# Kernel optimization log

Measured on AMD Instinct MI355X. Metric: run time of the kernel, lower is better.

Reference implementation:

```python
import jax, jax.numpy as jnp
import numpy as np

N, E, D_IN, HD, H = 50000, 800000, 768, 64, 4
HC = HD * H


def _gat(x, src, dst, etypes, lin_w, att_src, att_dst, edge_emb, lin_edge_w, att_edge,
         bias, res_w, res_b, ln_g, ln_b):
    # Faithful PyG GATConv (edge_dim, concat=True, add_self_loops=True with
    # fill_value='mean', negative_slope=0.2) + residual + LayerNorm. Eval mode: no dropout.
    n = x.shape[0]
    h, c = att_src.shape
    xs = (x @ lin_w).reshape(n, h, c)                      # [N,H,C]
    a_src = jnp.einsum('nhc,hc->nh', xs, att_src)          # [N,H]
    a_dst = jnp.einsum('nhc,hc->nh', xs, att_dst)
    eattr = edge_emb[etypes]                               # [E,ed]
    ones = jnp.ones((etypes.shape[0],), x.dtype)
    cnt = jax.ops.segment_sum(ones, dst, num_segments=n)
    # self-loop edge_attr = mean of incoming edge attrs per node (fill_value='mean')
    loop_attr = jax.ops.segment_sum(eattr, dst, num_segments=n) / jnp.maximum(cnt, 1.0)[:, None]
    loop = jnp.arange(n, dtype=src.dtype)
    src_a = jnp.concatenate([src, loop])
    dst_a = jnp.concatenate([dst, loop])
    e_all = jnp.concatenate([eattr, loop_attr], 0)
    a_edge = jnp.einsum('ehc,hc->eh', (e_all @ lin_edge_w).reshape(-1, h, c), att_edge)
    alpha = jax.nn.leaky_relu(a_src[src_a] + a_dst[dst_a] + a_edge, 0.2)   # [Ea,H]
    # edge softmax over incoming edges of each destination node
    amax = jax.ops.segment_max(alpha, dst_a, num_segments=n)
    ea = jnp.exp(alpha - amax[dst_a])
    denom = jax.ops.segment_sum(ea, dst_a, num_segments=n)
    w = ea / (denom[dst_a] + 1e-16)
    out = jax.ops.segment_sum(xs[src_a] * w[:, :, None], dst_a, num_segments=n)
    out = out.reshape(n, h * c) + bias + (x @ res_w + res_b)
    mu = out.mean(-1, keepdims=True)
    var = jnp.mean((out - mu) ** 2, -1, keepdims=True)
    return (out - mu) * jax.lax.rsqrt(var + 1e-5) * ln_g + ln_b


def _forward(features, positions,
             fe_w1, fe_b1, fe_w2, fe_b2, fe_pos_w, fe_pos_b, fe_type_emb, fe_out_w, fe_out_b,
             g1_lin_w, g1_att_src, g1_att_dst, g1_edge_emb, g1_lin_edge_w, g1_att_edge,
             g1_bias, g1_res_w, g1_res_b, g1_ln_g, g1_ln_b,
             g2_lin_w, g2_att_src, g2_att_dst, g2_edge_emb, g2_lin_edge_w, g2_att_edge,
             g2_bias, g2_res_w, g2_res_b, g2_ln_g, g2_ln_b,
             cls_w, cls_b,
             edge_index, aspect_indices, edge_types, node_types):
    # EnhancedFeatureExtractor (eval: dropout = identity)
    hfe = jax.nn.relu(features @ fe_w1 + fe_b1) @ fe_w2 + fe_b2
    hfe = hfe + fe_type_emb[node_types] + positions[:, None] @ fe_pos_w + fe_pos_b
    hfe = hfe @ fe_out_w + fe_out_b
    src, dst = edge_index[0], edge_index[1]
    hid = _gat(hfe, src, dst, edge_types, g1_lin_w, g1_att_src, g1_att_dst, g1_edge_emb,
               g1_lin_edge_w, g1_att_edge, g1_bias, g1_res_w, g1_res_b, g1_ln_g, g1_ln_b)
    hid = jax.nn.relu(hid)
    hid = _gat(hid, src, dst, edge_types, g2_lin_w, g2_att_src, g2_att_dst, g2_edge_emb,
               g2_lin_edge_w, g2_att_edge, g2_bias, g2_res_w, g2_res_b, g2_ln_g, g2_ln_b)
    return hid[aspect_indices] @ cls_w + cls_b


def setup_inputs() -> dict:
    key = jax.random.key(0)
    ks = jax.random.split(key, 40)
    d = {}
    d['features'] = jax.random.normal(ks[0], (N, D_IN), jnp.float32)
    d['edge_index'] = jax.random.randint(ks[1], (2, E), 0, N, jnp.int32)
    d['aspect_indices'] = jax.random.randint(ks[2], (4096,), 0, N, jnp.int32)
    d['edge_types'] = jax.random.randint(ks[3], (E,), 0, 4, jnp.int32)
    d['node_types'] = jax.random.randint(ks[4], (N,), 0, 3, jnp.int32)
    d['positions'] = jax.random.uniform(ks[5], (N,), jnp.float32)

    def rn(i, shape, s=0.05):
        return s * jax.random.normal(ks[i], shape, jnp.float32)

    d['fe_w1'] = rn(6, (D_IN, HD)); d['fe_b1'] = rn(7, (HD,))
    d['fe_w2'] = rn(8, (HD, HD));   d['fe_b2'] = rn(9, (HD,))
    d['fe_pos_w'] = rn(10, (1, HD)); d['fe_pos_b'] = rn(11, (HD,))
    d['fe_type_emb'] = rn(12, (3, HD))
    d['fe_out_w'] = rn(13, (HD, HD)); d['fe_out_b'] = rn(14, (HD,))
    d['g1_lin_w'] = rn(15, (HD, HC))
    d['g1_att_src'] = rn(16, (H, HD)); d['g1_att_dst'] = rn(17, (H, HD))
    d['g1_edge_emb'] = rn(18, (4, 4)); d['g1_lin_edge_w'] = rn(19, (4, HC))
    d['g1_att_edge'] = rn(20, (H, HD))
    d['g1_bias'] = rn(21, (HC,)); d['g1_res_w'] = rn(22, (HD, HC)); d['g1_res_b'] = rn(23, (HC,))
    d['g1_ln_g'] = jnp.ones((HC,), jnp.float32); d['g1_ln_b'] = jnp.zeros((HC,), jnp.float32)
    d['g2_lin_w'] = rn(24, (HC, HD))
    d['g2_att_src'] = rn(25, (1, HD)); d['g2_att_dst'] = rn(26, (1, HD))
    d['g2_edge_emb'] = rn(27, (4, 4)); d['g2_lin_edge_w'] = rn(28, (4, HD))
    d['g2_att_edge'] = rn(29, (1, HD))
    d['g2_bias'] = rn(30, (HD,)); d['g2_res_w'] = rn(31, (HC, HD)); d['g2_res_b'] = rn(32, (HD,))
    d['g2_ln_g'] = jnp.ones((HD,), jnp.float32); d['g2_ln_b'] = jnp.zeros((HD,), jnp.float32)
    d['cls_w'] = rn(33, (HD, 3)); d['cls_b'] = rn(34, (3,))
    return d


def reference(features, edge_index, aspect_indices, edge_types, node_types, positions,
              fe_w1, fe_b1, fe_w2, fe_b2, fe_pos_w, fe_pos_b, fe_type_emb, fe_out_w, fe_out_b,
              g1_lin_w, g1_att_src, g1_att_dst, g1_edge_emb, g1_lin_edge_w, g1_att_edge,
              g1_bias, g1_res_w, g1_res_b, g1_ln_g, g1_ln_b,
              g2_lin_w, g2_att_src, g2_att_dst, g2_edge_emb, g2_lin_edge_w, g2_att_edge,
              g2_bias, g2_res_w, g2_res_b, g2_ln_g, g2_ln_b,
              cls_w, cls_b):
    return _forward(features, positions,
                    fe_w1, fe_b1, fe_w2, fe_b2, fe_pos_w, fe_pos_b, fe_type_emb, fe_out_w, fe_out_b,
                    g1_lin_w, g1_att_src, g1_att_dst, g1_edge_emb, g1_lin_edge_w, g1_att_edge,
                    g1_bias, g1_res_w, g1_res_b, g1_ln_g, g1_ln_b,
                    g2_lin_w, g2_att_src, g2_att_dst, g2_edge_emb, g2_lin_edge_w, g2_att_edge,
                    g2_bias, g2_res_w, g2_res_b, g2_ln_g, g2_ln_b,
                    cls_w, cls_b,
                    edge_index, aspect_indices, edge_types, node_types)
```

## Files before the change

kernel.cpp:

```cpp
#include <hip/hip_runtime.h>


#define LRELU(x) ((x) > 0.f ? (x) : 0.2f * (x))

typedef __attribute__((ext_vector_type(8))) short short8;
typedef __attribute__((ext_vector_type(4))) float floatx4;

__device__ __forceinline__ unsigned short f2bf(float x) {
    union { float f; unsigned int u; } v; v.f = x;
    unsigned int r = (v.u + 0x7FFFu + ((v.u >> 16) & 1u)) >> 16;
    return (unsigned short)r;
}
__device__ __forceinline__ unsigned int cvtpk(float lo, float hi) {
    unsigned int r;
    asm("v_cvt_pk_bf16_f32 %0, %1, %2" : "=v"(r) : "v"(lo), "v"(hi));
    return r;
}
__device__ __forceinline__ float bflo(unsigned int u) {
    return __uint_as_float(u << 16);
}
__device__ __forceinline__ float bfhi(unsigned int u) {
    return __uint_as_float(u & 0xFFFF0000u);
}
__device__ __forceinline__ float bf1(unsigned short u) {
    return __uint_as_float(((unsigned int)u) << 16);
}

__global__ __launch_bounds__(256) void k_pre0(
    const float* __restrict__ e_emb1, const float* __restrict__ lew1,
    const float* __restrict__ ae1,
    const float* __restrict__ e_emb2, const float* __restrict__ lew2,
    const float* __restrict__ ae2,
    float* __restrict__ aet1, float* __restrict__ aet2,
    const float* __restrict__ w2, const float* __restrict__ outw,
    const float* __restrict__ b2, const float* __restrict__ posb,
    const float* __restrict__ outb, const float* __restrict__ temb,
    const float* __restrict__ posw,
    float* __restrict__ W2p, float* __restrict__ h0,
    float* __restrict__ tadd, float* __restrict__ padd)
{
    __shared__ float M1[16];
    __shared__ float M2[4];
    int t = threadIdx.x;
    if (blockIdx.x == 0) {
        if (t < 16) {
            int d = t >> 2, h = t & 3;
            float s = 0.f;
            for (int c = 0; c < 64; ++c) s += lew1[d * 256 + h * 64 + c] * ae1[h * 64 + c];
            M1[d * 4 + h] = s;
        }
        if (t < 4) {
            float s = 0.f;
            for (int c = 0; c < 64; ++c) s += lew2[t * 64 + c] * ae2[c];
            M2[t] = s;
        }
        __syncthreads();
        if (t < 16) {
            int ty = t >> 2, h = t & 3;
            float s = 0.f;
            for (int d = 0; d < 4; ++d) s += e_emb1[ty * 4 + d] * M1[d * 4 + h];
            aet1[ty * 4 + h] = s;
        }
        if (t < 4) {
            float s = 0.f;
            for (int d = 0; d < 4; ++d) s += e_emb2[t * 4 + d] * M2[d];
            aet2[t] = s;
        }
    } else {
        int i = t >> 2, jq = (t & 3) * 16;
        float a16[16];
#pragma unroll
        for (int u = 0; u < 16; ++u) a16[u] = 0.f;
        for (int k = 0; k < 64; ++k) {
            float a = w2[i * 64 + k];
            const float* op = outw + k * 64 + jq;
            float4 o0 = *(const float4*)op;
            float4 o1 = *(const float4*)(op + 4);
            float4 o2 = *(const float4*)(op + 8);
            float4 o3 = *(const float4*)(op + 12);
            a16[0] += a * o0.x;  a16[1] += a * o0.y;  a16[2] += a * o0.z;  a16[3] += a * o0.w;
            a16[4] += a * o1.x;  a16[5] += a * o1.y;  a16[6] += a * o1.z;  a16[7] += a * o1.w;
            a16[8] += a * o2.x;  a16[9] += a * o2.y;  a16[10] += a * o2.z; a16[11] += a * o2.w;
            a16[12] += a * o3.x; a16[13] += a * o3.y; a16[14] += a * o3.z; a16[15] += a * o3.w;
        }
#pragma unroll
        for (int u = 0; u < 16; ++u) W2p[i * 64 + jq + u] = a16[u];
        for (int e = t; e < 320; e += 256) {
            int g = e >> 6, j = e & 63;
            float s = 0.f;
            for (int k = 0; k < 64; ++k) {
                float v;
                if (g == 0) v = b2[k] + posb[k];
                else if (g <= 3) v = temb[(g - 1) * 64 + k];
                else v = posw[k];
                s += v * outw[k * 64 + j];
            }
            if (g == 0) h0[j] = s + outb[j];
            else if (g <= 3) tadd[(g - 1) * 64 + j] = s;
            else padd[j] = s;
        }
    }
}

__global__ __launch_bounds__(256) void k_bswz(
    const float* __restrict__ w1, const float* __restrict__ B1,
    const float* __restrict__ B2,
    unsigned short* __restrict__ out_fe1, unsigned short* __restrict__ out_p2)
{
    int idx = blockIdx.x * 256 + threadIdx.x;
    if (idx < 768 * 64) {
        int k = idx >> 6, col = idx & 63;
        int c = k >> 6, kl = k & 63, kg = kl >> 3, j = kl & 7;
        out_fe1[((c * 8 + kg) * 64 + col) * 8 + j] = f2bf(w1[k * 64 + col]);
    } else {
        int i2 = idx - 768 * 64;
        int k = i2 >> 7, col = i2 & 127;
        float v = (col < 64) ? B1[k * 64 + col] : B2[k * 64 + col - 64];
        int c = k >> 6, kl = k & 63, kg = kl >> 3, j = kl & 7;
        out_p2[((c * 8 + kg) * 128 + col) * 8 + j] = f2bf(v);
    }
}

__global__ __launch_bounds__(64) void k_fuse2(
    const float* __restrict__ W2p, const float* __restrict__ h0,
    const float* __restrict__ tadd, const float* __restrict__ padd,
    const float* __restrict__ lin_w, const float* __restrict__ res_w,
    const float* __restrict__ bias, const float* __restrict__ res_b,
    unsigned short* __restrict__ bz, float* __restrict__ C0,
    float* __restrict__ T, float* __restrict__ P)
{
    __shared__ float bcol[64];
    int c = blockIdx.x;
    int j = threadIdx.x;
    int cL = c & 255;
    const float* Bsrc = (c < 256) ? lin_w : res_w;
    float bv = Bsrc[j * 256 + cL];
    bcol[j] = bv;
    __syncthreads();
    float s = 0.f;
#pragma unroll 8
    for (int k = 0; k < 64; ++k) s += W2p[j * 64 + k] * bcol[k];
    int kg = j >> 3, jj = j & 7, ct = c >> 7, cl = c & 127;
    bz[((ct * 8 + kg) * 128 + cl) * 8 + jj] = f2bf(s);
    float pc = h0[j] * bv;
    float p0 = tadd[j] * bv, p1 = tadd[64 + j] * bv, p2 = tadd[128 + j] * bv;
    float pp = padd[j] * bv;
#pragma unroll
    for (int k = 32; k; k >>= 1) {
        pc += __shfl_xor(pc, k, 64); p0 += __shfl_xor(p0, k, 64);
        p1 += __shfl_xor(p1, k, 64); p2 += __shfl_xor(p2, k, 64);
        pp += __shfl_xor(pp, k, 64);
    }
    if (j == 0) {
        C0[c] = pc + ((c >= 256) ? (bias[cL] + res_b[cL]) : 0.f);
        T[c] = p0; T[512 + c] = p1; T[1024 + c] = p2;
        P[c] = pp;
    }
}

__global__ __launch_bounds__(256) void k_fe1(
    const float* __restrict__ feat, const unsigned short* __restrict__ bswz,
    const float* __restrict__ b1, unsigned short* __restrict__ t1b, int N)
{
    int t = threadIdx.x;
    int wv = t >> 6, lane = t & 63;
    int quad = lane >> 4, l16 = lane & 15;
    long rw = (long)blockIdx.x * 64 + wv * 16;
    long ra = rw + l16;
    if (ra >= N) ra = N - 1;
    const float* fbase = feat + ra * 768 + quad * 8;

    floatx4 acc[4];
#pragma unroll
    for (int i = 0; i < 4; ++i) acc[i] = (floatx4){0.f, 0.f, 0.f, 0.f};

    for (int ci = 0; ci < 12; ++ci) {
        const float* fc = fbase + ci * 64;
        short8 af[2];
#pragma unroll
        for (int s = 0; s < 2; ++s) {
            float4 x = *(const float4*)(fc + s * 32);
            float4 y = *(const float4*)(fc + s * 32 + 4);
            uint4 u = {cvtpk(x.x, x.y), cvtpk(x.z, x.w),
                       cvtpk(y.x, y.y), cvtpk(y.z, y.w)};
            af[s] = *(short8*)&u;
        }
#pragma unroll
        for (int s = 0; s < 2; ++s) {
            int kg = s * 4 + quad;
#pragma unroll
            for (int ct = 0; ct < 4; ++ct) {
                short8 bfrag = *(const short8*)&bswz[
                    ((ci * 8 + kg) * 64 + ct * 16 + l16) * 8];
                acc[ct] = __builtin_amdgcn_mfma_f32_16x16x32_bf16(
                    af[s], bfrag, acc[ct], 0, 0, 0);
            }
        }
    }
#pragma unroll
    for (int ct = 0; ct < 4; ++ct) {
        float bb = b1[ct * 16 + l16];
#pragma unroll
        for (int r = 0; r < 4; ++r) {
            long m = rw + quad * 4 + r;
            if (m < N)
                t1b[m * 64 + ct * 16 + l16] = f2bf(fmaxf(acc[ct][r] + bb, 0.f));
        }
    }
}

__global__ __launch_bounds__(256) void k_prep1(
    const unsigned short* __restrict__ A, const unsigned short* __restrict__ bswz,
    const float* __restrict__ C0, const float* __restrict__ T,
    const float* __restrict__ P, const int* __restrict__ ntypes,
    const float* __restrict__ pos,
    unsigned short* __restrict__ xsb, unsigned short* __restrict__ resp, int N)
{
    int t = threadIdx.x;
    int wv = t >> 6, lane = t & 63;
    int quad = lane >> 4, l16 = lane & 15;
    long rw = (long)blockIdx.x * 64 + wv * 16;
    int by = blockIdx.y;
    long ra = rw + l16;
    if (ra >= N) ra = N - 1;
    const unsigned short* abase = A + ra * 64 + quad * 8;

    floatx4 acc[8];
#pragma unroll
    for (int i = 0; i < 8; ++i) acc[i] = (floatx4){0.f, 0.f, 0.f, 0.f};

    short8 af[2];
    af[0] = *(const short8*)(abase);
    af[1] = *(const short8*)(abase + 32);
#pragma unroll
    for (int s = 0; s < 2; ++s) {
        int kg = s * 4 + quad;
#pragma unroll
        for (int c8 = 0; c8 < 8; ++c8) {
            short8 bfrag = *(const short8*)&bswz[
                ((by * 8 + kg) * 128 + c8 * 16 + l16) * 8];
            acc[c8] = __builtin_amdgcn_mfma_f32_16x16x32_bf16(
                af[s], bfrag, acc[c8], 0, 0, 0);
        }
    }
    int nta[4];
    float posa[4];
#pragma unroll
    for (int r = 0; r < 4; ++r) {
        long m = rw + quad * 4 + r;
        if (m < N) { nta[r] = ntypes[m]; posa[r] = pos[m]; }
        else       { nta[r] = 0; posa[r] = 0.f; }
    }
    bool isl = (by < 2);
    int cb = by * 128;
#pragma unroll
    for (int c8 = 0; c8 < 8; ++c8) {
        int gc = cb + c8 * 16 + l16;
        float c0 = C0[gc], pcf = P[gc];
#pragma unroll
        for (int r = 0; r < 4; ++r) {
            long m = rw + quad * 4 + r;
            if (m < N) {
                float val = acc[c8][r] + c0 + T[nta[r] * 512 + gc] + posa[r] * pcf;
                if (isl) xsb[m * 256 + gc] = f2bf(val);
                else     resp[m * 256 + gc - 256] = f2bf(val);
            }
        }
    }
}

__global__ __launch_bounds__(256) void k_prep2(
    const unsigned short* __restrict__ A, const unsigned short* __restrict__ bswz,
    const float* __restrict__ bias, const float* __restrict__ res_b,
    unsigned short* __restrict__ xsb, float* __restrict__ resp, int N)
{
    int t = threadIdx.x;
    int wv = t >> 6, lane = t & 63;
    int quad = lane >> 4, l16 = lane & 15;
    long rw = (long)blockIdx.x * 64 + wv * 16;
    long ra = rw + l16;
    if (ra >= N) ra = N - 1;
    const unsigned short* abase = A + ra * 256 + quad * 8;

    floatx4 acc[8];
#pragma unroll
    for (int i = 0; i < 8; ++i) acc[i] = (floatx4){0.f, 0.f, 0.f, 0.f};

    for (int ci = 0; ci < 4; ++ci) {
        short8 af[2];
        af[0] = *(const short8*)(abase + ci * 64);
        af[1] = *(const short8*)(abase + ci * 64 + 32);
#pragma unroll
        for (int s = 0; s < 2; ++s) {
            int kg = s * 4 + quad;
#pragma unroll
            for (int c8 = 0; c8 < 8; ++c8) {
                short8 bfrag = *(const short8*)&bswz[
                    ((ci * 8 + kg) * 128 + c8 * 16 + l16) * 8];
                acc[c8] = __builtin_amdgcn_mfma_f32_16x16x32_bf16(
                    af[s], bfrag, acc[c8], 0, 0, 0);
            }
        }
    }
#pragma unroll
    for (int c8 = 0; c8 < 8; ++c8) {
        int gc = c8 * 16 + l16;
        bool isl = gc < 64;
        float badd = isl ? 0.f : (bias[gc - 64] + res_b[gc - 64]);
#pragma unroll
        for (int r = 0; r < 4; ++r) {
            long m = rw + quad * 4 + r;
            if (m < N) {
                float val = acc[c8][r];
                if (isl) xsb[m * 64 + gc] = f2bf(val);
                else     resp[m * 64 + gc - 64] = val + badd;
            }
        }
    }
}

template<int H>
__global__ __launch_bounds__(256) void k_att(
    const unsigned short* __restrict__ xsb, const float* __restrict__ att_s,
    const float* __restrict__ att_d, float* __restrict__ a_src,
    float* __restrict__ a_dst, int N)
{
    int t = threadIdx.x;
    int wv = t >> 6, lane = t & 63;
    long n = (long)blockIdx.x * 4 + wv;
    if (n >= N) return;
    if (H == 4) {
        ushort4 u = *(const ushort4*)&xsb[n * 256 + lane * 4];
        float4 as = *(const float4*)&att_s[lane * 4];
        float4 ad = *(const float4*)&att_d[lane * 4];
        float x0 = bf1(u.x), x1 = bf1(u.y), x2 = bf1(u.z), x3 = bf1(u.w);
        float p = x0 * as.x + x1 * as.y + x2 * as.z + x3 * as.w;
        float q = x0 * ad.x + x1 * ad.y + x2 * ad.z + x3 * ad.w;
#pragma unroll
        for (int k = 8; k; k >>= 1) {
            p += __shfl_xor(p, k, 64);
            q += __shfl_xor(q, k, 64);
        }
        if ((lane & 15) == 0) {
            a_src[n * 4 + (lane >> 4)] = p;
            a_dst[n * 4 + (lane >> 4)] = q;
        }
    } else {
        float x = bf1(xsb[n * 64 + lane]);
        float p = x * att_s[lane];
        float q = x * att_d[lane];
#pragma unroll
        for (int k = 32; k; k >>= 1) {
            p += __shfl_xor(p, k, 64);
            q += __shfl_xor(q, k, 64);
        }
        if (lane == 0) { a_src[n] = p; a_dst[n] = q; }
    }
}

__global__ __launch_bounds__(256) void k_count(
    const int* __restrict__ dst, const int* __restrict__ et,
    int* __restrict__ cnt_t, int E)
{
    int e = blockIdx.x * 256 + threadIdx.x;
    if (e < E) atomicAdd(&cnt_t[dst[e] * 4 + et[e]], 1);
}

__global__ __launch_bounds__(256) void k_scan1(
    const int* __restrict__ cnt_t, int* __restrict__ row_off,
    int* __restrict__ blk_sums, int N)
{
    __shared__ int s[256];
    int t = threadIdx.x;
    int i = blockIdx.x * 256 + t;
    int v = 0;
    if (i < N) v = cnt_t[4 * i] + cnt_t[4 * i + 1] + cnt_t[4 * i + 2] + cnt_t[4 * i + 3];
    s[t] = v;
    __syncthreads();
    for (int off = 1; off < 256; off <<= 1) {
        int x = 0;
        if (t >= off) x = s[t - off];
        __syncthreads();
        s[t] += x;
        __syncthreads();
    }
    if (i < N) row_off[i] = s[t] - v;
    if (t == 255) blk_sums[blockIdx.x] = s[255];
}

__global__ __launch_bounds__(256) void k_scan2(int* __restrict__ blk_sums, int nb)
{
    __shared__ int s[256];
    int t = threadIdx.x;
    int v = (t < nb) ? blk_sums[t] : 0;
    s[t] = v;
    __syncthreads();
    for (int off = 1; off < 256; off <<= 1) {
        int x = 0;
        if (t >= off) x = s[t - off];
        __syncthreads();
        s[t] += x;
        __syncthreads();
    }
    if (t < nb) blk_sums[t] = s[t] - v;
}

__global__ __launch_bounds__(256) void k_scan3(
    int* __restrict__ row_off, int* __restrict__ cursor,
    const int* __restrict__ blk_sums, int N, int E)
{
    int t = threadIdx.x;
    int i = blockIdx.x * 256 + t;
    if (i < N) {
        int o = row_off[i] + blk_sums[blockIdx.x];
        row_off[i] = o;
        cursor[i] = o;
    }
    if (i == 0) row_off[N] = E;
}

__global__ __launch_bounds__(256) void k_scatter(
    const int* __restrict__ src, const int* __restrict__ dst,
    const int* __restrict__ et, int* __restrict__ cursor,
    int* __restrict__ csr_pack, int E)
{
    int e = blockIdx.x * 256 + threadIdx.x;
    if (e < E) {
        int d = dst[e];
        int pos = atomicAdd(&cursor[d], 1);
        csr_pack[pos] = src[e] | (et[e] << 28);
    }
}

__global__ __launch_bounds__(128) void k_gat1(
    const unsigned short* __restrict__ xs1b, const float* __restrict__ a_src,
    const float* __restrict__ a_dst, const int* __restrict__ row_off,
    const int* __restrict__ csr_pack,
    const int* __restrict__ cnt_t, const float* __restrict__ aet1,
    const float* __restrict__ ln_g, const float* __restrict__ ln_b,
    const unsigned short* __restrict__ res, unsigned short* __restrict__ out)
{
    __shared__ __align__(16) float4 ws[2][64];
    __shared__ float2 aetp[2][4];
    __shared__ float red[4];
    int n = blockIdx.x;
    int t = threadIdx.x;
    int w = t >> 6, c = t & 63;
    int lc = c & 15, g = c >> 4;
    int h0 = 2 * w;
    if (t < 8) {
        int w2 = t >> 2, ty = t & 3;
        aetp[w2][ty] = make_float2(aet1[ty * 4 + 2 * w2], aet1[ty * 4 + 2 * w2 + 1]);
    }
    int off = row_off[n], deg = row_off[n + 1] - off;
    float2 a_d = *(const float2*)&a_dst[n * 4 + h0];
    __syncthreads();
    float ael0 = 0.f, ael1 = 0.f;
    int degc = 0;
#pragma unroll
    for (int ty = 0; ty < 4; ++ty) {
        int ct = cnt_t[n * 4 + ty];
        degc += ct;
        float2 ae = aetp[w][ty];
        ael0 += (float)ct * ae.x;
        ael1 += (float)ct * ae.y;
    }
    float inv = (degc > 0) ? 1.f / (float)degc : 1.f;
    float2 a_s_self = *(const float2*)&a_src[n * 4 + h0];
    float al0 = a_s_self.x + a_d.x + ael0 * inv;
    float al1 = a_s_self.y + a_d.y + ael1 * inv;
    al0 = LRELU(al0); al1 = LRELU(al1);
    float wself0 = expf(al0), wself1 = expf(al1);

    int col0 = w * 128 + lc * 8;
    const unsigned short* xrow = xs1b + col0;
    float acc[8];
#pragma unroll
    for (int j = 0; j < 8; ++j) acc[j] = 0.f;
    float dp0 = 0.f, dp1 = 0.f;

    for (int base = 0; base < deg; base += 64) {
        int cnt = min(64, deg - base);
        float w0 = 0.f, w1 = 0.f;
        int s = 0;
        if (c < cnt) {
            int pk = csr_pack[off + base + c];
            s = pk & 0x0FFFFFFF;
            int ty = ((unsigned)pk) >> 28;
            float2 as2 = *(const float2*)&a_src[s * 4 + h0];
            float2 ae = aetp[w][ty];
            float a0 = as2.x + a_d.x + ae.x;
            float a1 = as2.y + a_d.y + ae.y;
            a0 = LRELU(a0); a1 = LRELU(a1);
            w0 = expf(a0); w1 = expf(a1);
        }
        dp0 += w0; dp1 += w1;
        ws[w][c] = make_float4(w0, w1, __int_as_float(s), 0.f);
        int cr = (cnt + 7) & ~7;
        for (int i = 0; i < cr; i += 8) {
#pragma unroll
            for (int u = 0; u < 2; ++u) {
                float4 p = ws[w][i + u * 4 + g];
                float wl = (lc < 8) ? p.x : p.y;
                uint4 q = *(const uint4*)&xrow[(long)__float_as_int(p.z) * 256];
                acc[0] += wl * bflo(q.x); acc[1] += wl * bfhi(q.x);
                acc[2] += wl * bflo(q.y); acc[3] += wl * bfhi(q.y);
                acc[4] += wl * bflo(q.z); acc[5] += wl * bfhi(q.z);
                acc[6] += wl * bflo(q.w); acc[7] += wl * bfhi(q.w);
            }
        }
    }
#pragma unroll
    for (int k = 32; k; k >>= 1) {
        dp0 += __shfl_xor(dp0, k, 64);
        dp1 += __shfl_xor(dp1, k, 64);
    }
#pragma unroll
    for (int j = 0; j < 8; ++j) {
        acc[j] += __shfl_xor(acc[j], 16, 64);
        acc[j] += __shfl_xor(acc[j], 32, 64);
    }
    uint4 us = *(const uint4*)&xrow[(long)n * 256];
    float wself_l = (lc < 8) ? wself0 : wself1;
    acc[0] += wself_l * bflo(us.x); acc[1] += wself_l * bfhi(us.x);
    acc[2] += wself_l * bflo(us.y); acc[3] += wself_l * bfhi(us.y);
    acc[4] += wself_l * bflo(us.z); acc[5] += wself_l * bfhi(us.z);
    acc[6] += wself_l * bflo(us.w); acc[7] += wself_l * bfhi(us.w);
    float dsum = ((lc < 8) ? dp0 + wself0 : dp1 + wself1) + 1e-16f;
    float rd = 1.f / dsum;
    uint4 ur = *(const uint4*)&res[(long)n * 256 + col0];
    float v[8];
    v[0] = acc[0] * rd + bflo(ur.x); v[1] = acc[1] * rd + bfhi(ur.x);
    v[2] = acc[2] * rd + bflo(ur.y); v[3] = acc[3] * rd + bfhi(ur.y);
    v[4] = acc[4] * rd + bflo(ur.z); v[5] = acc[5] * rd + bfhi(ur.z);
    v[6] = acc[6] * rd + bflo(ur.w); v[7] = acc[7] * rd + bfhi(ur.w);
    float s1 = 0.f, s2 = 0.f;
#pragma unroll
    for (int j = 0; j < 8; ++j) { s1 += v[j]; s2 += v[j] * v[j]; }
#pragma unroll
    for (int k = 32; k; k >>= 1) {
        s1 += __shfl_xor(s1, k, 64);
        s2 += __shfl_xor(s2, k, 64);
    }
    if (c == 0) { red[w] = s1 * 0.25f; red[2 + w] = s2 * 0.25f; }
    __syncthreads();
    float mu = (red[0] + red[1]) * (1.f / 256.f);
    float var = (red[2] + red[3]) * (1.f / 256.f) - mu * mu;
    float rs = rsqrtf(var + 1e-5f);
    if (g == 0) {
        float4 lg0 = *(const float4*)&ln_g[col0];
        float4 lg1 = *(const float4*)&ln_g[col0 + 4];
        float4 lb0 = *(const float4*)&ln_b[col0];
        float4 lb1 = *(const float4*)&ln_b[col0 + 4];
        float y[8];
        y[0] = fmaxf((v[0] - mu) * rs * lg0.x + lb0.x, 0.f);
        y[1] = fmaxf((v[1] - mu) * rs * lg0.y + lb0.y, 0.f);
        y[2] = fmaxf((v[2] - mu) * rs * lg0.z + lb0.z, 0.f);
        y[3] = fmaxf((v[3] - mu) * rs * lg0.w + lb0.w, 0.f);
        y[4] = fmaxf((v[4] - mu) * rs * lg1.x + lb1.x, 0.f);
        y[5] = fmaxf((v[5] - mu) * rs * lg1.y + lb1.y, 0.f);
        y[6] = fmaxf((v[6] - mu) * rs * lg1.z + lb1.z, 0.f);
        y[7] = fmaxf((v[7] - mu) * rs * lg1.w + lb1.w, 0.f);
        uint4 o;
        o.x = cvtpk(y[0], y[1]); o.y = cvtpk(y[2], y[3]);
        o.z = cvtpk(y[4], y[5]); o.w = cvtpk(y[6], y[7]);
        *(uint4*)&out[(long)n * 256 + col0] = o;
    }
}

__global__ __launch_bounds__(64) void k_gat2(
    const unsigned short* __restrict__ xs2b, const float* __restrict__ a_src,
    const float* __restrict__ a_dst, const int* __restrict__ row_off,
    const int* __restrict__ csr_pack,
    const int* __restrict__ cnt_t, const float* __restrict__ aet2,
    const float* __restrict__ ln_g, const float* __restrict__ ln_b,
    float* io)
{
    __shared__ __align__(8) float2 ws[64];
    __shared__ float aetl[4];
    int n = blockIdx.x;
    int c = threadIdx.x;
    int lc = c & 15, g = c >> 4;
    if (c < 4) aetl[c] = aet2[c];
    int off = row_off[n], deg = row_off[n + 1] - off;
    float a_d = a_dst[n];
    float ael = 0.f;
    int degc = 0;
#pragma unroll
    for (int ty = 0; ty < 4; ++ty) {
        int ct = cnt_t[n * 4 + ty];
        degc += ct;
        ael += (float)ct * aet2[ty];
    }
    ael *= (degc > 0 ? 1.f / (float)degc : 1.f);
    float al = a_src[n] + a_d + ael;
    al = LRELU(al);
    float wself = expf(al);

    int colb = lc * 4;
    const unsigned short* xrow = xs2b + colb;
    float acc[4] = {0.f, 0.f, 0.f, 0.f};
    float dp = 0.f;
    for (int base = 0; base < deg; base += 64) {
        int cnt = min(64, deg - base);
        float we = 0.f;
        int s = 0;
        if (c < cnt) {
            int pk = csr_pack[off + base + c];
            s = pk & 0x0FFFFFFF;
            int ty = ((unsigned)pk) >> 28;
            float a = a_src[s] + a_d + aetl[ty];
            a = LRELU(a);
            we = expf(a);
        }
        dp += we;
        ws[c] = make_float2(we, __int_as_float(s));
        int cr = (cnt + 7) & ~7;
        for (int i = 0; i < cr; i += 8) {
#pragma unroll
            for (int u = 0; u < 2; ++u) {
                float2 p = ws[i + u * 4 + g];
                uint2 q = *(const uint2*)&xrow[(long)__float_as_int(p.y) * 64];
                acc[0] += p.x * bflo(q.x); acc[1] += p.x * bfhi(q.x);
                acc[2] += p.x * bflo(q.y); acc[3] += p.x * bfhi(q.y);
            }
        }
    }
#pragma unroll
    for (int k = 32; k; k >>= 1) dp += __shfl_xor(dp, k, 64);
#pragma unroll
    for (int j = 0; j < 4; ++j) {
        acc[j] += __shfl_xor(acc[j], 16, 64);
        acc[j] += __shfl_xor(acc[j], 32, 64);
    }
    uint2 us = *(const uint2*)&xrow[(long)n * 64];
    acc[0] += wself * bflo(us.x); acc[1] += wself * bfhi(us.x);
    acc[2] += wself * bflo(us.y); acc[3] += wself * bfhi(us.y);
    float dsum = dp + wself + 1e-16f;
    float rd = 1.f / dsum;
    float4 r = *(const float4*)&io[(long)n * 64 + colb];
    float v[4];
    v[0] = acc[0] * rd + r.x; v[1] = acc[1] * rd + r.y;
    v[2] = acc[2] * rd + r.z; v[3] = acc[3] * rd + r.w;
    float s1 = v[0] + v[1] + v[2] + v[3];
    float s2 = v[0] * v[0] + v[1] * v[1] + v[2] * v[2] + v[3] * v[3];
#pragma unroll
    for (int k = 32; k; k >>= 1) {
        s1 += __shfl_xor(s1, k, 64);
        s2 += __shfl_xor(s2, k, 64);
    }
    float mu = s1 * (1.f / 256.f);
    float var = s2 * (1.f / 256.f) - mu * mu;
    float rs = rsqrtf(var + 1e-5f);
    if (g == 0) {
        float4 lg = *(const float4*)&ln_g[colb];
        float4 lb = *(const float4*)&ln_b[colb];
        float4 y;
        y.x = (v[0] - mu) * rs * lg.x + lb.x;
        y.y = (v[1] - mu) * rs * lg.y + lb.y;
        y.z = (v[2] - mu) * rs * lg.z + lb.z;
        y.w = (v[3] - mu) * rs * lg.w + lb.w;
        *(float4*)&io[(long)n * 64 + colb] = y;
    }
}

__global__ __launch_bounds__(256) void k_cls(
    const float* __restrict__ hid2, const int* __restrict__ asp,
    const float* __restrict__ w, const float* __restrict__ b,
    float* __restrict__ out)
{
    int g = blockIdx.x * 256 + threadIdx.x;
    int i = g / 3, j = g - i * 3;
    int a = asp[i];
    float acc = b[j];
#pragma unroll 8
    for (int cc = 0; cc < 64; ++cc) acc += hid2[(long)a * 64 + cc] * w[cc * 3 + j];
    out[i * 3 + j] = acc;
}

extern "C" void kernel_launch(void* const* d_in, const int* in_sizes, int n_in,
                              void* d_out, int out_size, void* d_ws, size_t ws_size,
                              hipStream_t stream)
{
    const float* features    = (const float*)d_in[0];
    const int*   edge_index  = (const int*)d_in[1];
    const int*   aspect      = (const int*)d_in[2];
    const int*   etypes      = (const int*)d_in[3];
    const int*   ntypes      = (const int*)d_in[4];
    const float* pos         = (const float*)d_in[5];
    const float* fe_w1       = (const float*)d_in[6];
    const float* fe_b1       = (const float*)d_in[7];
    const float* fe_w2       = (const float*)d_in[8];
    const float* fe_b2       = (const float*)d_in[9];
    const float* fe_pos_w    = (const float*)d_in[10];
    const float* fe_pos_b    = (const float*)d_in[11];
    const float* fe_type_emb = (const float*)d_in[12];
    const float* fe_out_w    = (const float*)d_in[13];
    const float* fe_out_b    = (const float*)d_in[14];
    const float* g1_lin_w    = (const float*)d_in[15];
    const float* g1_att_src  = (const float*)d_in[16];
    const float* g1_att_dst  = (const float*)d_in[17];
    const float* g1_edge_emb = (const float*)d_in[18];
    const float* g1_lin_edge = (const float*)d_in[19];
    const float* g1_att_edge = (const float*)d_in[20];
    const float* g1_bias     = (const float*)d_in[21];
    const float* g1_res_w    = (const float*)d_in[22];
    const float* g1_res_b    = (const float*)d_in[23];
    const float* g1_ln_g     = (const float*)d_in[24];
    const float* g1_ln_b     = (const float*)d_in[25];
    const float* g2_lin_w    = (const float*)d_in[26];
    const float* g2_att_src  = (const float*)d_in[27];
    const float* g2_att_dst  = (const float*)d_in[28];
    const float* g2_edge_emb = (const float*)d_in[29];
    const float* g2_lin_edge = (const float*)d_in[30];
    const float* g2_att_edge = (const float*)d_in[31];
    const float* g2_bias     = (const float*)d_in[32];
    const float* g2_res_w    = (const float*)d_in[33];
    const float* g2_res_b    = (const float*)d_in[34];
    const float* g2_ln_g     = (const float*)d_in[35];
    const float* g2_ln_b     = (const float*)d_in[36];
    const float* cls_w       = (const float*)d_in[37];
    const float* cls_b       = (const float*)d_in[38];

    const int N = in_sizes[0] / 768;
    const int E = in_sizes[1] / 2;
    const int* src = edge_index;
    const int* dst = edge_index + E;

    char* wsb = (char*)d_ws;
    size_t off = 0;
    auto alloc = [&](size_t bytes) -> char* {
        char* p = wsb + off;
        off += (bytes + 255) & ~(size_t)255;
        return p;
    };
    unsigned short* t1b  = (unsigned short*)alloc((size_t)N * 64 * 2);
    unsigned short* xs1b = (unsigned short*)alloc((size_t)N * 256 * 2);
    unsigned short* xs2b = (unsigned short*)alloc((size_t)N * 64 * 2);
    unsigned short* hid1b= (unsigned short*)alloc((size_t)N * 256 * 2);
    unsigned short* rp1  = (unsigned short*)alloc((size_t)N * 256 * 2);
    float* rp2     = (float*)alloc((size_t)N * 64 * 4);
    float* a_src1  = (float*)alloc((size_t)N * 4 * 4);
    float* a_dst1  = (float*)alloc((size_t)N * 4 * 4);
    float* a_src2  = (float*)alloc((size_t)N * 4);
    float* a_dst2  = (float*)alloc((size_t)N * 4);
    int*   cnt_t   = (int*)alloc((size_t)N * 4 * 4);
    int*   row_off = (int*)alloc((size_t)(N + 1) * 4);
    int*   cursor  = (int*)alloc((size_t)N * 4);
    int*   blk     = (int*)alloc(1024);
    int*   csr_pack= (int*)alloc((size_t)E * 4);
    float* aet1    = (float*)alloc(64);
    float* aet2    = (float*)alloc(64);
    unsigned short* bz_fe1 = (unsigned short*)alloc(768 * 64 * 2);
    unsigned short* bz_p1  = (unsigned short*)alloc(64 * 512 * 2);
    unsigned short* bz_p2  = (unsigned short*)alloc(256 * 128 * 2);
    float* W2p     = (float*)alloc(64 * 64 * 4);
    float* h0v     = (float*)alloc(64 * 4);
    float* taddv   = (float*)alloc(192 * 4);
    float* paddv   = (float*)alloc(64 * 4);
    float* C0t     = (float*)alloc(512 * 4);
    float* Tt      = (float*)alloc(3 * 512 * 4);
    float* Pt      = (float*)alloc(512 * 4);

    hipMemsetAsync(cnt_t, 0, (size_t)N * 4 * 4, stream);

    int mb = (N + 63) / 64;
    int ab = (N + 3) / 4;

    k_pre0<<<2, 256, 0, stream>>>(g1_edge_emb, g1_lin_edge, g1_att_edge,
                                  g2_edge_emb, g2_lin_edge, g2_att_edge, aet1, aet2,
                                  fe_w2, fe_out_w, fe_b2, fe_pos_b, fe_out_b,
                                  fe_type_emb, fe_pos_w, W2p, h0v, taddv, paddv);
    k_bswz<<<320, 256, 0, stream>>>(fe_w1, g2_lin_w, g2_res_w, bz_fe1, bz_p2);
    k_fuse2<<<512, 64, 0, stream>>>(W2p, h0v, taddv, paddv, g1_lin_w, g1_res_w,
                                    g1_bias, g1_res_b, bz_p1, C0t, Tt, Pt);
    k_fe1<<<mb, 256, 0, stream>>>(features, bz_fe1, fe_b1, t1b, N);
    k_prep1<<<dim3(mb, 4), 256, 0, stream>>>(
        t1b, bz_p1, C0t, Tt, Pt, ntypes, pos, xs1b, rp1, N);
    k_att<4><<<ab, 256, 0, stream>>>(xs1b, g1_att_src, g1_att_dst, a_src1, a_dst1, N);
    int eblk = (E + 255) / 256;
    int nb = (N + 255) / 256;
    k_count<<<eblk, 256, 0, stream>>>(dst, etypes, cnt_t, E);
    k_scan1<<<nb, 256, 0, stream>>>(cnt_t, row_off, blk, N);
    k_scan2<<<1, 256, 0, stream>>>(blk, nb);
    k_scan3<<<nb, 256, 0, stream>>>(row_off, cursor, blk, N, E);
    k_scatter<<<eblk, 256, 0, stream>>>(src, dst, etypes, cursor, csr_pack, E);
    k_gat1<<<N, 128, 0, stream>>>(xs1b, a_src1, a_dst1, row_off, csr_pack,
                                  cnt_t, aet1, g1_ln_g, g1_ln_b, rp1, hid1b);
    k_prep2<<<mb, 256, 0, stream>>>(hid1b, bz_p2, g2_bias, g2_res_b, xs2b, rp2, N);
    k_att<1><<<ab, 256, 0, stream>>>(xs2b, g2_att_src, g2_att_dst, a_src2, a_dst2, N);
    k_gat2<<<N, 64, 0, stream>>>(xs2b, a_src2, a_dst2, row_off, csr_pack,
                                 cnt_t, aet2, g2_ln_g, g2_ln_b, rp2);
    k_cls<<<(out_size + 255) / 256, 256, 0, stream>>>(rp2, aspect, cls_w, cls_b,
                                                      (float*)d_out);
}
```

Baseline: 620.9 us.

## Fuse attention-score epilogues, precompute edge weights in scatter, merge small kernels

Attention logits are now computed in the GEMM epilogues of k_prep1/k_prep2, which removes the separate k_att passes. The scan2 kernel is folded into scan3 through a per-block reduction of block sums. k_pre0 and k_bswz become one launch. k_scatter now precomputes the exp'd layer-1 edge weights into a new wbuf ordered like the CSR, so k_gat1 reads them instead of gathering a_src. k_gat2 processes two nodes per block. This cuts launches and redundant gathers, but adds a 12.8MB weight buffer to write and read, and one redundant reduction of block sums per scan3 block.

```diff
diff --git a/kernel.cpp b/kernel.cpp
--- a/kernel.cpp
+++ b/kernel.cpp
@@ -26,7 +26,7 @@
     return __uint_as_float(((unsigned int)u) << 16);
 }
 
-__global__ __launch_bounds__(256) void k_pre0(
+__global__ __launch_bounds__(256) void k_front(
     const float* __restrict__ e_emb1, const float* __restrict__ lew1,
     const float* __restrict__ ae1,
     const float* __restrict__ e_emb2, const float* __restrict__ lew2,
@@ -37,12 +37,16 @@
     const float* __restrict__ outb, const float* __restrict__ temb,
     const float* __restrict__ posw,
     float* __restrict__ W2p, float* __restrict__ h0,
-    float* __restrict__ tadd, float* __restrict__ padd)
+    float* __restrict__ tadd, float* __restrict__ padd,
+    const float* __restrict__ w1, const float* __restrict__ B1,
+    const float* __restrict__ B2,
+    unsigned short* __restrict__ out_fe1, unsigned short* __restrict__ out_p2)
 {
     __shared__ float M1[16];
     __shared__ float M2[4];
     int t = threadIdx.x;
-    if (blockIdx.x == 0) {
+    int b = blockIdx.x;
+    if (b == 0) {
         if (t < 16) {
             int d = t >> 2, h = t & 3;
             float s = 0.f;
@@ -66,7 +70,7 @@
             for (int d = 0; d < 4; ++d) s += e_emb2[t * 4 + d] * M2[d];
             aet2[t] = s;
         }
-    } else {
+    } else if (b == 1) {
         int i = t >> 2, jq = (t & 3) * 16;
         float a16[16];
 #pragma unroll
@@ -99,25 +103,19 @@
             else if (g <= 3) tadd[(g - 1) * 64 + j] = s;
             else padd[j] = s;
         }
-    }
-}
-
-__global__ __launch_bounds__(256) void k_bswz(
-    const float* __restrict__ w1, const float* __restrict__ B1,
-    const float* __restrict__ B2,
-    unsigned short* __restrict__ out_fe1, unsigned short* __restrict__ out_p2)
-{
-    int idx = blockIdx.x * 256 + threadIdx.x;
-    if (idx < 768 * 64) {
-        int k = idx >> 6, col = idx & 63;
-        int c = k >> 6, kl = k & 63, kg = kl >> 3, j = kl & 7;
-        out_fe1[((c * 8 + kg) * 64 + col) * 8 + j] = f2bf(w1[k * 64 + col]);
     } else {
-        int i2 = idx - 768 * 64;
-        int k = i2 >> 7, col = i2 & 127;
-        float v = (col < 64) ? B1[k * 64 + col] : B2[k * 64 + col - 64];
-        int c = k >> 6, kl = k & 63, kg = kl >> 3, j = kl & 7;
-        out_p2[((c * 8 + kg) * 128 + col) * 8 + j] = f2bf(v);
+        int idx = (b - 2) * 256 + t;
+        if (idx < 768 * 64) {
+            int k = idx >> 6, col = idx & 63;
+            int c = k >> 6, kl = k & 63, kg = kl >> 3, j = kl & 7;
+            out_fe1[((c * 8 + kg) * 64 + col) * 8 + j] = f2bf(w1[k * 64 + col]);
+        } else {
+            int i2 = idx - 768 * 64;
+            int k = i2 >> 7, col = i2 & 127;
+            float v = (col < 64) ? B1[k * 64 + col] : B2[k * 64 + col - 64];
+            int c = k >> 6, kl = k & 63, kg = kl >> 3, j = kl & 7;
+            out_p2[((c * 8 + kg) * 128 + col) * 8 + j] = f2bf(v);
+        }
     }
 }
 
@@ -214,7 +212,9 @@
     const float* __restrict__ C0, const float* __restrict__ T,
     const float* __restrict__ P, const int* __restrict__ ntypes,
     const float* __restrict__ pos,
-    unsigned short* __restrict__ xsb, unsigned short* __restrict__ resp, int N)
+    const float* __restrict__ att_s, const float* __restrict__ att_d,
+    unsigned short* __restrict__ xsb, unsigned short* __restrict__ resp,
+    float* __restrict__ a_src, float* __restrict__ a_dst, int N)
 {
     int t = threadIdx.x;
     int wv = t >> 6, lane = t & 63;
@@ -253,26 +253,54 @@
     }
     bool isl = (by < 2);
     int cb = by * 128;
+    float ps[2][4] = {{0.f,0.f,0.f,0.f},{0.f,0.f,0.f,0.f}};
+    float pd[2][4] = {{0.f,0.f,0.f,0.f},{0.f,0.f,0.f,0.f}};
 #pragma unroll
     for (int c8 = 0; c8 < 8; ++c8) {
         int gc = cb + c8 * 16 + l16;
         float c0 = C0[gc], pcf = P[gc];
+        float as = 0.f, ad = 0.f;
+        if (isl) { as = att_s[gc]; ad = att_d[gc]; }
+        int hh = c8 >> 2;
 #pragma unroll
         for (int r = 0; r < 4; ++r) {
             long m = rw + quad * 4 + r;
+            float val = acc[c8][r] + c0 + T[nta[r] * 512 + gc] + posa[r] * pcf;
             if (m < N) {
-                float val = acc[c8][r] + c0 + T[nta[r] * 512 + gc] + posa[r] * pcf;
                 if (isl) xsb[m * 256 + gc] = f2bf(val);
                 else     resp[m * 256 + gc - 256] = f2bf(val);
             }
-        }
+            ps[hh][r] += val * as;
+            pd[hh][r] += val * ad;
+        }
+    }
+    if (isl) {
+#pragma unroll
+        for (int h = 0; h < 2; ++h)
+#pragma unroll
+            for (int r = 0; r < 4; ++r) {
+                float a = ps[h][r], b = pd[h][r];
+#pragma unroll
+                for (int k = 1; k < 16; k <<= 1) {
+                    a += __shfl_xor(a, k, 64);
+                    b += __shfl_xor(b, k, 64);
+                }
+                long m = rw + quad * 4 + r;
+                if (l16 == 0 && m < N) {
+                    int h4 = by * 2 + h;
+                    a_src[m * 4 + h4] = a;
+                    a_dst[m * 4 + h4] = b;
+                }
+            }
     }
 }
 
 __global__ __launch_bounds__(256) void k_prep2(
     const unsigned short* __restrict__ A, const unsigned short* __restrict__ bswz,
     const float* __restrict__ bias, const float* __restrict__ res_b,
-    unsigned short* __restrict__ xsb, float* __restrict__ resp, int N)
+    const float* __restrict__ att_s, const float* __restrict__ att_d,
+    unsigned short* __restrict__ xsb, float* __restrict__ resp,
+    float* __restrict__ a_src, float* __restrict__ a_dst, int N)
 {
     int t = threadIdx.x;
     int wv = t >> 6, lane = t & 63;
@@ -302,59 +330,35 @@
             }
         }
     }
+    float ps[4] = {0.f,0.f,0.f,0.f}, pd[4] = {0.f,0.f,0.f,0.f};
 #pragma unroll
     for (int c8 = 0; c8 < 8; ++c8) {
         int gc = c8 * 16 + l16;
         bool isl = gc < 64;
         float badd = isl ? 0.f : (bias[gc - 64] + res_b[gc - 64]);
+        float as = isl ? att_s[gc] : 0.f;
+        float ad = isl ? att_d[gc] : 0.f;
 #pragma unroll
         for (int r = 0; r < 4; ++r) {
             long m = rw + quad * 4 + r;
+            float val = acc[c8][r];
             if (m < N) {
-                float val = acc[c8][r];
                 if (isl) xsb[m * 64 + gc] = f2bf(val);
                 else     resp[m * 64 + gc - 64] = val + badd;
             }
-        }
-    }
-}
-
-template<int H>
-__global__ __launch_bounds__(256) void k_att(
-    const unsigned short* __restrict__ xsb, const float* __restrict__ att_s,
-    const float* __restrict__ att_d, float* __restrict__ a_src,
-    float* __restrict__ a_dst, int N)
-{
-    int t = threadIdx.x;
-    int wv = t >> 6, lane = t & 63;
-    long n = (long)blockIdx.x * 4 + wv;
-    if (n >= N) return;
-    if (H == 4) {
-        ushort4 u = *(const ushort4*)&xsb[n * 256 + lane * 4];
-        float4 as = *(const float4*)&att_s[lane * 4];
-        float4 ad = *(const float4*)&att_d[lane * 4];
-        float x0 = bf1(u.x), x1 = bf1(u.y), x2 = bf1(u.z), x3 = bf1(u.w);
-        float p = x0 * as.x + x1 * as.y + x2 * as.z + x3 * as.w;
-        float q = x0 * ad.x + x1 * ad.y + x2 * ad.z + x3 * ad.w;
-#pragma unroll
-        for (int k = 8; k; k >>= 1) {
-            p += __shfl_xor(p, k, 64);
-            q += __shfl_xor(q, k, 64);
-        }
-        if ((lane & 15) == 0) {
-            a_src[n * 4 + (lane >> 4)] = p;
-            a_dst[n * 4 + (lane >> 4)] = q;
-        }
-    } else {
-        float x = bf1(xsb[n * 64 + lane]);
-        float p = x * att_s[lane];
-        float q = x * att_d[lane];
-#pragma unroll
-        for (int k = 32; k; k >>= 1) {
-            p += __shfl_xor(p, k, 64);
-            q += __shfl_xor(q, k, 64);
-        }
-        if (lane == 0) { a_src[n] = p; a_dst[n] = q; }
+            if (isl) { ps[r] += val * as; pd[r] += val * ad; }
+        }
+    }
+#pragma unroll
+    for (int r = 0; r < 4; ++r) {
+        float a = ps[r], b = pd[r];
+#pragma unroll
+        for (int k = 1; k < 16; k <<= 1) {
+            a += __shfl_xor(a, k, 64);
+            b += __shfl_xor(b, k, 64);
+        }
+        long m = rw + quad * 4 + r;
+        if (l16 == 0 && m < N) { a_src[m] = a; a_dst[m] = b; }
     }
 }
 
@@ -388,31 +392,23 @@
     if (t == 255) blk_sums[blockIdx.x] = s[255];
 }
 
-__global__ __launch_bounds__(256) void k_scan2(int* __restrict__ blk_sums, int nb)
-{
-    __shared__ int s[256];
-    int t = threadIdx.x;
-    int v = (t < nb) ? blk_sums[t] : 0;
-    s[t] = v;
-    __syncthreads();
-    for (int off = 1; off < 256; off <<= 1) {
-        int x = 0;
-        if (t >= off) x = s[t - off];
-        __syncthreads();
-        s[t] += x;
-        __syncthreads();
-    }
-    if (t < nb) blk_sums[t] = s[t] - v;
-}
-
 __global__ __launch_bounds__(256) void k_scan3(
     int* __restrict__ row_off, int* __restrict__ cursor,
     const int* __restrict__ blk_sums, int N, int E)
 {
+    __shared__ int s[256];
     int t = threadIdx.x;
-    int i = blockIdx.x * 256 + t;
+    int bid = blockIdx.x;
+    s[t] = (t < bid) ? blk_sums[t] : 0;
+    __syncthreads();
+    for (int off = 128; off; off >>= 1) {
+        if (t < off) s[t] += s[t + off];
+        __syncthreads();
+    }
+    int prev = s[0];
+    int i = bid * 256 + t;
     if (i < N) {
-        int o = row_off[i] + blk_sums[blockIdx.x];
+        int o = row_off[i] + prev;
         row_off[i] = o;
         cursor[i] = o;
     }
@@ -422,20 +418,34 @@
 __global__ __launch_bounds__(256) void k_scatter(
     const int* __restrict__ src, const int* __restrict__ dst,
     const int* __restrict__ et, int* __restrict__ cursor,
-    int* __restrict__ csr_pack, int E)
+    int* __restrict__ csr_pack,
+    const float* __restrict__ a_src, const float* __restrict__ a_dst,
+    const float* __restrict__ aet1, float* __restrict__ wbuf, int E)
 {
     int e = blockIdx.x * 256 + threadIdx.x;
     if (e < E) {
         int d = dst[e];
+        int s = src[e];
+        int ty = et[e];
         int pos = atomicAdd(&cursor[d], 1);
-        csr_pack[pos] = src[e] | (et[e] << 28);
+        csr_pack[pos] = s | (ty << 28);
+        float4 as4 = *(const float4*)&a_src[s * 4];
+        float4 ad4 = *(const float4*)&a_dst[d * 4];
+        float4 ae = *(const float4*)&aet1[ty * 4];
+        float a0 = as4.x + ad4.x + ae.x;
+        float a1 = as4.y + ad4.y + ae.y;
+        float a2 = as4.z + ad4.z + ae.z;
+        float a3 = as4.w + ad4.w + ae.w;
+        a0 = LRELU(a0); a1 = LRELU(a1); a2 = LRELU(a2); a3 = LRELU(a3);
+        float4 w4 = make_float4(expf(a0), expf(a1), expf(a2), expf(a3));
+        *(float4*)&wbuf[(long)pos * 4] = w4;
     }
 }
 
 __global__ __launch_bounds__(128) void k_gat1(
     const unsigned short* __restrict__ xs1b, const float* __restrict__ a_src,
     const float* __restrict__ a_dst, const int* __restrict__ row_off,
-    const int* __restrict__ csr_pack,
+    const int* __restrict__ csr_pack, const float* __restrict__ wbuf,
     const int* __restrict__ cnt_t, const float* __restrict__ aet1,
     const float* __restrict__ ln_g, const float* __restrict__ ln_b,
     const unsigned short* __restrict__ res, unsigned short* __restrict__ out)
@@ -484,15 +494,11 @@
         float w0 = 0.f, w1 = 0.f;
         int s = 0;
         if (c < cnt) {
-            int pk = csr_pack[off + base + c];
+            int idx = off + base + c;
+            int pk = csr_pack[idx];
             s = pk & 0x0FFFFFFF;
-            int ty = ((unsigned)pk) >> 28;
-            float2 as2 = *(const float2*)&a_src[s * 4 + h0];
-            float2 ae = aetp[w][ty];
-            float a0 = as2.x + a_d.x + ae.x;
-            float a1 = as2.y + a_d.y + ae.y;
-            a0 = LRELU(a0); a1 = LRELU(a1);
-            w0 = expf(a0); w1 = expf(a1);
+            float2 wv = *(const float2*)&wbuf[(long)idx * 4 + 2 * w];
+            w0 = wv.x; w1 = wv.y;
         }
         dp0 += w0; dp1 += w1;
         ws[w][c] = make_float4(w0, w1, __int_as_float(s), 0.f);
@@ -568,20 +574,19 @@
     }
 }
 
-__global__ __launch_bounds__(64) void k_gat2(
+__global__ __launch_bounds__(128) void k_gat2(
     const unsigned short* __restrict__ xs2b, const float* __restrict__ a_src,
     const float* __restrict__ a_dst, const int* __restrict__ row_off,
     const int* __restrict__ csr_pack,
     const int* __restrict__ cnt_t, const float* __restrict__ aet2,
     const float* __restrict__ ln_g, const float* __restrict__ ln_b,
-    float* io)
-{
-    __shared__ __align__(8) float2 ws[64];
-    __shared__ float aetl[4];
-    int n = blockIdx.x;
-    int c = threadIdx.x;
+    float* io, int N)
+{
+    __shared__ __align__(8) float2 ws[2][64];
+    int v_ = threadIdx.x >> 6, c = threadIdx.x & 63;
+    int n = blockIdx.x * 2 + v_;
+    if (n >= N) return;
     int lc = c & 15, g = c >> 4;
-    if (c < 4) aetl[c] = aet2[c];
     int off = row_off[n], deg = row_off[n + 1] - off;
     float a_d = a_dst[n];
     float ael = 0.f;
@@ -609,17 +614,17 @@
             int pk = csr_pack[off + base + c];
             s = pk & 0x0FFFFFFF;
             int ty = ((unsigned)pk) >> 28;
-            float a = a_src[s] + a_d + aetl[ty];
+            float a = a_src[s] + a_d + aet2[ty];
             a = LRELU(a);
             we = expf(a);
         }
         dp += we;
-        ws[c] = make_float2(we, __int_as_float(s));
+        ws[v_][c] = make_float2(we, __int_as_float(s));
         int cr = (cnt + 7) & ~7;
         for (int i = 0; i < cr; i += 8) {
 #pragma unroll
             for (int u = 0; u < 2; ++u) {
-                float2 p = ws[i + u * 4 + g];
+                float2 p = ws[v_][i + u * 4 + g];
                 uint2 q = *(const uint2*)&xrow[(long)__float_as_int(p.y) * 64];
                 acc[0] += p.x * bflo(q.x); acc[1] += p.x * bfhi(q.x);
                 acc[2] += p.x * bflo(q.y); acc[3] += p.x * bfhi(q.y);
@@ -749,6 +754,7 @@
     int*   cursor  = (int*)alloc((size_t)N * 4);
     int*   blk     = (int*)alloc(1024);
     int*   csr_pack= (int*)alloc((size_t)E * 4);
+    float* wbuf    = (float*)alloc((size_t)E * 4 * 4);
     float* aet1    = (float*)alloc(64);
     float* aet2    = (float*)alloc(64);
     unsigned short* bz_fe1 = (unsigned short*)alloc(768 * 64 * 2);
@@ -765,32 +771,34 @@
     hipMemsetAsync(cnt_t, 0, (size_t)N * 4 * 4, stream);
 
     int mb = (N + 63) / 64;
-    int ab = (N + 3) / 4;
-
-    k_pre0<<<2, 256, 0, stream>>>(g1_edge_emb, g1_lin_edge, g1_att_edge,
-                                  g2_edge_emb, g2_lin_edge, g2_att_edge, aet1, aet2,
-                                  fe_w2, fe_out_w, fe_b2, fe_pos_b, fe_out_b,
-                                  fe_type_emb, fe_pos_w, W2p, h0v, taddv, paddv);
-    k_bswz<<<320, 256, 0, stream>>>(fe_w1, g2_lin_w, g2_res_w, bz_fe1, bz_p2);
+    int eblk = (E + 255) / 256;
+    int nb = (N + 255) / 256;
+
+    k_front<<<322, 256, 0, stream>>>(
+        g1_edge_emb, g1_lin_edge, g1_att_edge,
+        g2_edge_emb, g2_lin_edge, g2_att_edge, aet1, aet2,
+        fe_w2, fe_out_w, fe_b2, fe_pos_b, fe_out_b, fe_type_emb, fe_pos_w,
+        W2p, h0v, taddv, paddv,
+        fe_w1, g2_lin_w, g2_res_w, bz_fe1, bz_p2);
     k_fuse2<<<512, 64, 0, stream>>>(W2p, h0v, taddv, paddv, g1_lin_w, g1_res_w,
                                     g1_bias, g1_res_b, bz_p1, C0t, Tt, Pt);
+    k_count<<<eblk, 256, 0, stream>>>(dst, etypes, cnt_t, E);
+    k_scan1<<<nb, 256, 0, stream>>>(cnt_t, row_off, blk, N);
+    k_scan3<<<nb, 256, 0, stream>>>(row_off, cursor, blk, N, E);
     k_fe1<<<mb, 256, 0, stream>>>(features, bz_fe1, fe_b1, t1b, N);
     k_prep1<<<dim3(mb, 4), 256, 0, stream>>>(
-        t1b, bz_p1, C0t, Tt, Pt, ntypes, pos, xs1b, rp1, N);
-    k_att<4><<<ab, 256, 0, stream>>>(xs1b, g1_att_src, g1_att_dst, a_src1, a_dst1, N);
-    int eblk = (E + 255) / 256;
-    int nb = (N + 255) / 256;
-    k_count<<<eblk, 256, 0, stream>>>(dst, etypes, cnt_t, E);
-    k_scan1<<<nb, 256, 0, stream>>>(cnt_t, row_off, blk, N);
-    k_scan2<<<1, 256, 0, stream>>>(blk, nb);
-    k_scan3<<<nb, 256, 0, stream>>>(row_off, cursor, blk, N, E);
-    k_scatter<<<eblk, 256, 0, stream>>>(src, dst, etypes, cursor, csr_pack, E);
-    k_gat1<<<N, 128, 0, stream>>>(xs1b, a_src1, a_dst1, row_off, csr_pack,
+        t1b, bz_p1, C0t, Tt, Pt, ntypes, pos, g1_att_src, g1_att_dst,
+        xs1b, rp1, a_src1, a_dst1, N);
+    k_scatter<<<eblk, 256, 0, stream>>>(src, dst, etypes, cursor, csr_pack,
+                                        a_src1, a_dst1, aet1, wbuf, E);
+    k_gat1<<<N, 128, 0, stream>>>(xs1b, a_src1, a_dst1, row_off, csr_pack, wbuf,
                                   cnt_t, aet1, g1_ln_g, g1_ln_b, rp1, hid1b);
-    k_prep2<<<mb, 256, 0, stream>>>(hid1b, bz_p2, g2_bias, g2_res_b, xs2b, rp2, N);
-    k_att<1><<<ab, 256, 0, stream>>>(xs2b, g2_att_src, g2_att_dst, a_src2, a_dst2, N);
-    k_gat2<<<N, 64, 0, stream>>>(xs2b, a_src2, a_dst2, row_off, csr_pack,
-                                 cnt_t, aet2, g2_ln_g, g2_ln_b, rp2);
+    k_prep2<<<mb, 256, 0, stream>>>(hid1b, bz_p2, g2_bias, g2_res_b,
+                                    g2_att_src, g2_att_dst, xs2b, rp2,
+                                    a_src2, a_dst2, N);
+    k_gat2<<<(N + 1) / 2, 128, 0, stream>>>(xs2b, a_src2, a_dst2, row_off,
+                                            csr_pack, cnt_t, aet2,
+                                            g2_ln_g, g2_ln_b, rp2, N);
     k_cls<<<(out_size + 255) / 256, 256, 0, stream>>>(rp2, aspect, cls_w, cls_b,
                                                       (float*)d_out);
 }
```

Result: faster. 605.0 us (-2.6%).
